# Optimization experiments

Hardware: AMD Instinct MI355X
Metric: run time of the kernel (lower is better)

## Reference

```python
import jax, jax.numpy as jnp
import numpy as np

N_EMBD = 1024
N_HEAD = 16
HEAD_DIM = N_EMBD // N_HEAD
D_FF = 4 * N_EMBD


def dyt(x, alpha, gamma, beta):
    # Dynamic Tanh normalizer: gamma * tanh(alpha * x) + beta
    return gamma * jnp.tanh(x * alpha) + beta


def setup_inputs() -> dict:
    key = jax.random.key(0)
    ks = jax.random.split(key, 9)
    C, F = N_EMBD, D_FF
    s = 0.02
    return {
        "x": jax.random.normal(ks[0], (2, 2048, C), dtype=jnp.float32),
        "alpha": jnp.ones((1,), jnp.float32) * 0.5,
        "gamma": jnp.ones((C,), jnp.float32),
        "beta": jnp.zeros((C,), jnp.float32),
        "w_attn": jax.random.normal(ks[1], (C, 3 * C), jnp.float32) * s,
        "b_attn": jnp.zeros((3 * C,), jnp.float32),
        "w_proj": jax.random.normal(ks[2], (C, C), jnp.float32) * s,
        "b_proj": jnp.zeros((C,), jnp.float32),
        "w_fc": jax.random.normal(ks[3], (C, F), jnp.float32) * s,
        "b_fc": jnp.zeros((F,), jnp.float32),
        "w_fc2": jax.random.normal(ks[4], (F, C), jnp.float32) * s,
        "b_fc2": jnp.zeros((C,), jnp.float32),
    }


def reference(x, alpha, gamma, beta, w_attn, b_attn, w_proj, b_proj,
              w_fc, b_fc, w_fc2, b_fc2):
    B, T, C = x.shape
    H, D = N_HEAD, HEAD_DIM

    # --- attention branch (pre-norm with DyT) ---
    h = dyt(x, alpha, gamma, beta)
    qkv = h @ w_attn + b_attn                      # [B,T,3C]
    q, k, v = jnp.split(qkv, 3, axis=-1)
    q = q.reshape(B, T, H, D).transpose(0, 2, 1, 3)  # [B,H,T,D]
    k = k.reshape(B, T, H, D).transpose(0, 2, 1, 3)
    v = v.reshape(B, T, H, D).transpose(0, 2, 1, 3)

    scores = jnp.einsum('bhqd,bhkd->bhqk', q, k) / jnp.sqrt(jnp.asarray(D, x.dtype))
    causal = jnp.tril(jnp.ones((T, T), bool))
    scores = jnp.where(causal[None, None], scores, -jnp.inf)
    attn = jax.nn.softmax(scores, axis=-1)          # [B,H,T,T]
    out = jnp.einsum('bhqk,bhkd->bhqd', attn, v)    # [B,H,T,D]
    out = out.transpose(0, 2, 1, 3).reshape(B, T, C)
    x = x + (out @ w_proj + b_proj)

    # --- MLP branch (pre-norm with same DyT params, as in source) ---
    h2 = dyt(x, alpha, gamma, beta)
    mlp = jax.nn.gelu(h2 @ w_fc + b_fc, approximate=False) @ w_fc2 + b_fc2
    return x + mlp
```

## Files before the change

### kernel.cpp

```cpp
#include <hip/hip_runtime.h>
#include <cstdint>
#include <cstddef>

typedef __bf16 bf16;
typedef __bf16 bf16x8 __attribute__((ext_vector_type(8)));
typedef __bf16 bf16x4 __attribute__((ext_vector_type(4)));
typedef float f32x4 __attribute__((ext_vector_type(4)));

#define DEVI __device__ __forceinline__

DEVI void gload_lds16(const bf16* g, bf16* l) {
    __builtin_amdgcn_global_load_lds(
        (const __attribute__((address_space(1))) void*)(const void*)g,
        (__attribute__((address_space(3))) void*)(void*)l, 16, 0, 0);
}

DEVI float fast_tanh(float y) {
    float t = __builtin_amdgcn_exp2f(2.88539008f * y);
    return 1.f - 2.f * __builtin_amdgcn_rcpf(1.f + t);
}

__global__ void conv_all_kernel(const float* __restrict__ wa, const float* __restrict__ wp,
                                const float* __restrict__ wfc, const float* __restrict__ wfc2,
                                bf16* __restrict__ ta, bf16* __restrict__ tp,
                                bf16* __restrict__ tfc, bf16* __restrict__ tfc2) {
    __shared__ float tile[64][65];
    int bid = blockIdx.x;
    const float* W; bf16* Wt; int K, N, nx;
    if (bid < 768)        { W = wa;   Wt = ta;   K = 1024; N = 3072; nx = 48; }
    else if (bid < 1024)  { bid -= 768;  W = wp;   Wt = tp;   K = 1024; N = 1024; nx = 16; }
    else if (bid < 2048)  { bid -= 1024; W = wfc;  Wt = tfc;  K = 1024; N = 4096; nx = 64; }
    else                  { bid -= 2048; W = wfc2; Wt = tfc2; K = 4096; N = 1024; nx = 16; }
    const int n0 = (bid % nx) * 64;
    const int k0 = (bid / nx) * 64;
    const int tid = threadIdx.x;
    const int c  = tid & 63;
    const int r4 = tid >> 6;
#pragma unroll
    for (int r = 0; r < 64; r += 4)
        tile[r + r4][c] = W[(size_t)(k0 + r + r4) * N + n0 + c];
    __syncthreads();
#pragma unroll
    for (int r = 0; r < 64; r += 4)
        Wt[(size_t)(n0 + r + r4) * K + k0 + c] = (bf16)tile[c][r + r4];
}

__global__ void dyt_kernel(const float* __restrict__ x, const float* __restrict__ alpha,
                           const float* __restrict__ gamma, const float* __restrict__ beta,
                           bf16* __restrict__ h, int total) {
    int i4 = (blockIdx.x * 256 + threadIdx.x) * 4;
    if (i4 >= total) return;
    float a = alpha[0];
    float4 xv = *(const float4*)&x[i4];
    int c = i4 & 1023;
    float4 g  = *(const float4*)&gamma[c];
    float4 bt = *(const float4*)&beta[c];
    bf16x4 o;
    o[0] = (bf16)(g.x * fast_tanh(xv.x * a) + bt.x);
    o[1] = (bf16)(g.y * fast_tanh(xv.y * a) + bt.y);
    o[2] = (bf16)(g.z * fast_tanh(xv.z * a) + bt.z);
    o[3] = (bf16)(g.w * fast_tanh(xv.w * a) + bt.w);
    *(bf16x4*)&h[i4] = o;
}

__global__ void reduce4_kernel(const bf16* __restrict__ p, const float* __restrict__ bias,
                               const bf16* __restrict__ x2b, float* __restrict__ out,
                               int total) {
    int i4 = (blockIdx.x * 256 + threadIdx.x) * 4;
    if (i4 >= total) return;
    bf16x4 q0 = *(const bf16x4*)&p[i4];
    bf16x4 q1 = *(const bf16x4*)&p[(size_t)total + i4];
    bf16x4 q2 = *(const bf16x4*)&p[(size_t)2 * total + i4];
    bf16x4 q3 = *(const bf16x4*)&p[(size_t)3 * total + i4];
    bf16x4 rr = *(const bf16x4*)&x2b[i4];
    int c = i4 & 1023;
    float4 bb = *(const float4*)&bias[c];
    float4 o;
    o.x = (float)q0[0] + (float)q1[0] + (float)q2[0] + (float)q3[0] + (float)rr[0] + bb.x;
    o.y = (float)q0[1] + (float)q1[1] + (float)q2[1] + (float)q3[1] + (float)rr[1] + bb.y;
    o.z = (float)q0[2] + (float)q1[2] + (float)q2[2] + (float)q3[2] + (float)rr[2] + bb.z;
    o.w = (float)q0[3] + (float)q1[3] + (float)q2[3] + (float)q3[3] + (float)rr[3] + bb.w;
    *(float4*)&out[i4] = o;
}

__global__ void reduce2b_dyt_kernel(const bf16* __restrict__ p, const float* __restrict__ bias,
                                    const float* __restrict__ x,
                                    bf16* __restrict__ x2b, bf16* __restrict__ hout,
                                    const float* __restrict__ alpha,
                                    const float* __restrict__ gamma,
                                    const float* __restrict__ beta, int total) {
    int i4 = (blockIdx.x * 256 + threadIdx.x) * 4;
    if (i4 >= total) return;
    float a = alpha[0];
    bf16x4 p0 = *(const bf16x4*)&p[i4];
    bf16x4 p1 = *(const bf16x4*)&p[(size_t)total + i4];
    float4 r  = *(const float4*)&x[i4];
    int c = i4 & 1023;
    float4 bb = *(const float4*)&bias[c];
    float4 g  = *(const float4*)&gamma[c];
    float4 bt = *(const float4*)&beta[c];
    float4 v;
    v.x = (float)p0[0] + (float)p1[0] + r.x + bb.x;
    v.y = (float)p0[1] + (float)p1[1] + r.y + bb.y;
    v.z = (float)p0[2] + (float)p1[2] + r.z + bb.z;
    v.w = (float)p0[3] + (float)p1[3] + r.w + bb.w;
    bf16x4 xo;
    xo[0] = (bf16)v.x; xo[1] = (bf16)v.y; xo[2] = (bf16)v.z; xo[3] = (bf16)v.w;
    *(bf16x4*)&x2b[i4] = xo;
    bf16x4 o;
    o[0] = (bf16)(g.x * fast_tanh(v.x * a) + bt.x);
    o[1] = (bf16)(g.y * fast_tanh(v.y * a) + bt.y);
    o[2] = (bf16)(g.z * fast_tanh(v.z * a) + bt.z);
    o[3] = (bf16)(g.w * fast_tanh(v.w * a) + bt.w);
    *(bf16x4*)&hout[i4] = o;
}

template<int OP>
__global__ void gemm_kernel(const bf16* __restrict__ A, const bf16* __restrict__ Wt,
                            const float* __restrict__ bias, const float* resid,
                            float* outf, bf16* outb,
                            const float* __restrict__ alpha_p,
                            const float* __restrict__ gamma,
                            const float* __restrict__ beta,
                            int M, int N, int K, int lda, int ldb) {
    __shared__ bf16 As[2][128 * 32];
    __shared__ bf16 Bs[2][128 * 32];
    const int tid  = threadIdx.x;
    const int lane = tid & 63;
    const int w    = tid >> 6;
    const int wr   = w >> 1, wc = w & 1;

    const int nwgx = gridDim.x;
    const int nwg  = gridDim.x * gridDim.y;
    const int orig = blockIdx.y * nwgx + blockIdx.x;
    const int cpx  = nwg >> 3;
    const int swz  = (orig & 7) * cpx + (orig >> 3);
    const int bm = (swz / nwgx) * 128;
    const int bn = (swz % nwgx) * 128;
    const int kz = blockIdx.z * K;

    f32x4 acc[4][4] = {};

    const int srow = tid >> 2;
    const int sgrp = ((tid & 3) ^ ((srow >> 1) & 3)) * 8;
    const bf16* a0 = A  + (size_t)(bm + srow) * lda + kz + sgrp;
    const bf16* a1 = a0 + (size_t)64 * lda;
    const bf16* b0 = Wt + (size_t)(bn + srow) * ldb + kz + sgrp;
    const bf16* b1 = b0 + (size_t)64 * ldb;

    auto stage = [&](int buf) {
        gload_lds16(a0, &As[buf][tid * 8]);
        gload_lds16(a1, &As[buf][2048 + tid * 8]);
        gload_lds16(b0, &Bs[buf][tid * 8]);
        gload_lds16(b1, &Bs[buf][2048 + tid * 8]);
        a0 += 32; a1 += 32; b0 += 32; b1 += 32;
    };

    const int lh = lane >> 4, lm = lane & 15;
    const int arow = wr * 64 + lm;
    const int brow = wc * 64 + lm;
    const int gsw = (lh ^ ((lm >> 1) & 3)) * 8;

    stage(0);
    __syncthreads();

    const int nk = K >> 5;
    for (int kt = 0; kt < nk; ++kt) {
        const int cur = kt & 1;
        if (kt + 1 < nk) stage(cur ^ 1);
        bf16x8 af[4], bfr[4];
#pragma unroll
        for (int i = 0; i < 4; i++)
            af[i] = *(const bf16x8*)&As[cur][(arow + i * 16) * 32 + gsw];
#pragma unroll
        for (int i = 0; i < 4; i++)
            bfr[i] = *(const bf16x8*)&Bs[cur][(brow + i * 16) * 32 + gsw];
#pragma unroll
        for (int i = 0; i < 4; i++)
#pragma unroll
            for (int j = 0; j < 4; j++)
                acc[i][j] = __builtin_amdgcn_mfma_f32_16x16x32_bf16(af[i], bfr[j], acc[i][j], 0, 0, 0);
        __syncthreads();
    }

#pragma unroll
    for (int i = 0; i < 4; i++) {
        const int row0 = bm + wr * 64 + i * 16 + lh * 4;
#pragma unroll
        for (int jf = 0; jf < 4; jf++) {
            const int col = bn + wc * 64 + jf * 16 + lm;
            const float bval = (OP == 5) ? 0.f : bias[col];
#pragma unroll
            for (int r = 0; r < 4; r++) {
                const int row = row0 + r;
                const size_t idx = (size_t)row * N + col;
                float v = acc[i][jf][r] + bval;
                if (OP == 0) {
                    const float qs = (col < 1024) ? 0.18033688011f : 1.0f;
                    outb[idx] = (bf16)(v * qs);
                } else {
                    outb[(size_t)blockIdx.z * M * N + idx] = (bf16)v;
                }
            }
        }
    }
}

template<int OP>
__global__ void __launch_bounds__(512, 2)
gemm256_kernel(const bf16* __restrict__ A, const bf16* __restrict__ Wt,
               const float* __restrict__ bias,
               bf16* __restrict__ outb, bf16* __restrict__ outpb,
               int M, int N, int K, int lda, int ldb) {
    __shared__ bf16 As[2][256][64];
    __shared__ bf16 Bs[2][256][64];
    const int tid  = threadIdx.x;
    const int lane = tid & 63;
    const int w    = tid >> 6;
    const int wr   = w >> 2;
    const int wcn  = w & 3;
    const int lh = lane >> 4, lm = lane & 15;

    const int nwgx = gridDim.x;
    const int nwg  = gridDim.x * gridDim.y;
    const int orig = blockIdx.y * nwgx + blockIdx.x;
    const int cpx  = nwg >> 3;
    const int swz  = (orig & 7) * cpx + (orig >> 3);
    const int bm = (swz / nwgx) * 256;
    const int bn = (swz % nwgx) * 256;
    const int kz = blockIdx.z * K;

    f32x4 acc[8][4] = {};

    const int srow = tid >> 3;
    const int sgr  = ((tid & 7) ^ (srow & 7)) * 8;
    const bf16* aSrc = A  + (size_t)(bm + srow) * lda + kz + sgr;
    const bf16* bSrc = Wt + (size_t)(bn + srow) * ldb + kz + sgr;

    auto STAGE = [&](int b, int kt) {
#pragma unroll
        for (int l = 0; l < 4; ++l)
            gload_lds16(aSrc + (size_t)(l * 64) * lda + kt * 64,
                        &As[b][0][0] + (l * 512 + tid) * 8);
#pragma unroll
        for (int l = 0; l < 4; ++l)
            gload_lds16(bSrc + (size_t)(l * 64) * ldb + kt * 64,
                        &Bs[b][0][0] + (l * 512 + tid) * 8);
    };

    auto COMPUTE2 = [&](int b) {
        bf16x8 bfr[2][2][2];
#pragma unroll
        for (int half = 0; half < 2; ++half) {
            bf16x8 af[4][2];
#pragma unroll
            for (int mf = 0; mf < 4; ++mf) {
                const int row = wr * 128 + (half * 4 + mf) * 16 + lm;
                const int sw = row & 7;
#pragma unroll
                for (int ks = 0; ks < 2; ++ks)
                    af[mf][ks] = *(const bf16x8*)&As[b][row][((ks * 4 + lh) ^ sw) * 8];
            }
            if (half == 0) {
#pragma unroll
                for (int qn = 0; qn < 2; ++qn)
#pragma unroll
                    for (int nf = 0; nf < 2; ++nf) {
                        const int row = wcn * 64 + (qn * 2 + nf) * 16 + lm;
                        const int sw = row & 7;
#pragma unroll
                        for (int ks = 0; ks < 2; ++ks)
                            bfr[qn][nf][ks] = *(const bf16x8*)&Bs[b][row][((ks * 4 + lh) ^ sw) * 8];
                    }
            }
            __builtin_amdgcn_s_setprio(1);
#pragma unroll
            for (int ks = 0; ks < 2; ++ks)
#pragma unroll
                for (int qn = 0; qn < 2; ++qn)
#pragma unroll
                    for (int mf = 0; mf < 4; ++mf)
#pragma unroll
                        for (int nf = 0; nf < 2; ++nf)
                            acc[half * 4 + mf][qn * 2 + nf] = __builtin_amdgcn_mfma_f32_16x16x32_bf16(
                                af[mf][ks], bfr[qn][nf][ks], acc[half * 4 + mf][qn * 2 + nf], 0, 0, 0);
            __builtin_amdgcn_s_setprio(0);
        }
    };

    const int nk = K >> 6;
    STAGE(0, 0);
    STAGE(1, 1);
    asm volatile("s_waitcnt vmcnt(8)" ::: "memory");
    __builtin_amdgcn_s_barrier();
    __builtin_amdgcn_sched_barrier(0);

    for (int kt = 0; kt < nk; kt += 2) {
        COMPUTE2(0);
        __builtin_amdgcn_s_barrier();
        if (kt + 2 < nk) {
            STAGE(0, kt + 2);
            asm volatile("s_waitcnt vmcnt(8)" ::: "memory");
        } else {
            asm volatile("s_waitcnt vmcnt(0)" ::: "memory");
        }
        __builtin_amdgcn_s_barrier();
        __builtin_amdgcn_sched_barrier(0);
        COMPUTE2(1);
        __builtin_amdgcn_s_barrier();
        if (kt + 3 < nk) {
            STAGE(1, kt + 3);
            asm volatile("s_waitcnt vmcnt(8)" ::: "memory");
        } else if (kt + 2 < nk) {
            asm volatile("s_waitcnt vmcnt(0)" ::: "memory");
        }
        __builtin_amdgcn_s_barrier();
        __builtin_amdgcn_sched_barrier(0);
    }

#pragma unroll
    for (int mf = 0; mf < 8; ++mf) {
        const int row0 = bm + wr * 128 + mf * 16 + lh * 4;
#pragma unroll
        for (int nf = 0; nf < 4; ++nf) {
            const int col = bn + wcn * 64 + nf * 16 + lm;
            const float bval = (OP == 4) ? 0.f : bias[col];
#pragma unroll
            for (int r = 0; r < 4; ++r) {
                const size_t idx = (size_t)(row0 + r) * N + col;
                float v = acc[mf][nf][r] + bval;
                if (OP == 2) {
                    float xc = v * (1.f + 0.044715f * v * v);
                    float g = v * __builtin_amdgcn_rcpf(
                        1.f + __builtin_amdgcn_exp2f(-2.30220795f * xc));
                    outb[idx] = (bf16)g;
                } else {
                    outpb[(size_t)blockIdx.z * M * N + idx] = (bf16)v;
                }
            }
        }
    }
}

__global__ void __launch_bounds__(256, 2)
attn_kernel(const bf16* __restrict__ qkv, bf16* __restrict__ out) {
    const int j  = blockIdx.x;
    const int bh = blockIdx.y;
    const int b = bh >> 4, h = bh & 15;
    const int tid = threadIdx.x, lane = tid & 63, w = tid >> 6;
    const int T = 2048;
    const size_t C3 = 3072;
    const bf16* qb = qkv + (size_t)b * T * C3 + h * 64;
    const bf16* kb = qb + 1024;
    const bf16* vb = qb + 2048;

    __shared__ bf16 Ks[2][64][64];
    __shared__ bf16 Vt[2][64][72];
    __shared__ bf16 Pl[2][4][16][72];

    const int tA = j, tB = 31 - j;
    const int qA = tA * 64 + w * 16;
    const int qB = tB * 64 + w * 16;
    const int lm = lane & 15;
    const int lh = lane >> 4;

    bf16x8 qfA0, qfA1, qfB0, qfB1;
    {
        size_t qo = (size_t)(qA + lm) * C3 + lh * 8;
        qfA0 = *(const bf16x8*)&qb[qo];
        qfA1 = *(const bf16x8*)&qb[qo + 32];
        qo = (size_t)(qB + lm) * C3 + lh * 8;
        qfB0 = *(const bf16x8*)&qb[qo];
        qfB1 = *(const bf16x8*)&qb[qo + 32];
    }
    f32x4 accA[4] = {}, accB[4] = {};
    float lA = 0.f, lB = 0.f;

    const int nt = tB + 1;
    const int sg = tid & 7;
    const int sq = tid >> 3;
    bf16x8 rv[4];

    const int krow = tid >> 3;
    const int kcb  = tid & 7;
    const int kcbs = (kcb ^ (krow & 7)) * 8;
    auto stageK = [&](int buf, int k0) {
        gload_lds16(&kb[(size_t)(k0 + krow) * C3 + kcbs],      &Ks[buf][0][0]  + tid * 8);
        gload_lds16(&kb[(size_t)(k0 + 32 + krow) * C3 + kcbs], &Ks[buf][32][0] + tid * 8);
    };
    auto loadV = [&](int k0) {
        if (tid < 128) {
#pragma unroll
            for (int i = 0; i < 4; ++i)
                rv[i] = *(const bf16x8*)&vb[(size_t)(k0 + sq * 4 + i) * C3 + sg * 8];
        }
    };
    auto writeV = [&](int buf) {
        if (tid < 128) {
            const int cbase = ((((sq >> 1) ^ sg) & 7) << 3) + ((sq & 1) << 2);
#pragma unroll
            for (int e = 0; e < 8; ++e) {
                bf16x4 wv;
                wv[0] = rv[0][e]; wv[1] = rv[1][e]; wv[2] = rv[2][e]; wv[3] = rv[3][e];
                *(bf16x4*)&Vt[buf][sg * 8 + e][cbase] = wv;
            }
        }
    };

    auto softmax_pv = [&](f32x4 (&s)[4], f32x4 (&acc)[4], float& lS,
                          int qg, bool diag, int k0, int slot, bf16x8 (&vf)[2][4]) {
        if (diag) {
#pragma unroll
            for (int f = 0; f < 4; ++f)
#pragma unroll
                for (int r = 0; r < 4; ++r) {
                    const int kgl = k0 + f * 16 + lh * 4 + r;
                    s[f][r] = (kgl > qg) ? -1e30f : s[f][r];
                }
        }
        float rs = 0.f;
#pragma unroll
        for (int f = 0; f < 4; ++f) {
            bf16x4 pw;
#pragma unroll
            for (int r = 0; r < 4; ++r) {
                const float pv = __builtin_amdgcn_exp2f(s[f][r]);
                rs += pv;
                pw[r] = (bf16)pv;
            }
            *(bf16x4*)&Pl[slot][w][lm][f * 16 + lh * 4] = pw;
        }
        __builtin_amdgcn_s_setprio(1);
#pragma unroll
        for (int kk = 0; kk < 2; ++kk) {
            bf16x8 pa = *(const bf16x8*)&Pl[slot][w][lm][kk * 32 + lh * 8];
#pragma unroll
            for (int df = 0; df < 4; ++df)
                acc[df] = __builtin_amdgcn_mfma_f32_16x16x32_bf16(vf[kk][df], pa, acc[df], 0, 0, 0);
        }
        __builtin_amdgcn_s_setprio(0);
        rs += __shfl_xor(rs, 16);
        rs += __shfl_xor(rs, 32);
        lS += rs;
    };

    stageK(0, 0);
    loadV(0);
    writeV(0);
    __syncthreads();

    for (int kt = 0; kt < nt; ++kt) {
        const int k0 = kt * 64;
        const int buf = kt & 1;
        const bool hasNext = (kt + 1 < nt);
        if (hasNext) {
            stageK(buf ^ 1, k0 + 64);
            loadV(k0 + 64);
        }

        bf16x8 kf[4][2];
#pragma unroll
        for (int f = 0; f < 4; ++f) {
            const int row = f * 16 + lm;
            const int sw = (row & 7);
            kf[f][0] = *(const bf16x8*)&Ks[buf][row][(lh ^ sw) * 8];
            kf[f][1] = *(const bf16x8*)&Ks[buf][row][((lh + 4) ^ sw) * 8];
        }
        bf16x8 vf[2][4];
#pragma unroll
        for (int kk = 0; kk < 2; ++kk)
#pragma unroll
            for (int df = 0; df < 4; ++df) {
                const int dr = df * 16 + lm;
                vf[kk][df] = *(const bf16x8*)&Vt[buf][dr][(((4 * kk + lh) ^ ((dr >> 3) & 7)) << 3)];
            }

        const bool actA = (kt <= tA);
        f32x4 sA[4], sB[4];
        __builtin_amdgcn_s_setprio(1);
#pragma unroll
        for (int f = 0; f < 4; ++f) {
            f32x4 z = {};
            z = __builtin_amdgcn_mfma_f32_16x16x32_bf16(kf[f][0], qfB0, z, 0, 0, 0);
            z = __builtin_amdgcn_mfma_f32_16x16x32_bf16(kf[f][1], qfB1, z, 0, 0, 0);
            sB[f] = z;
        }
        if (actA) {
#pragma unroll
            for (int f = 0; f < 4; ++f) {
                f32x4 z = {};
                z = __builtin_amdgcn_mfma_f32_16x16x32_bf16(kf[f][0], qfA0, z, 0, 0, 0);
                z = __builtin_amdgcn_mfma_f32_16x16x32_bf16(kf[f][1], qfA1, z, 0, 0, 0);
                sA[f] = z;
            }
        }
        __builtin_amdgcn_s_setprio(0);

        if (actA)
            softmax_pv(sA, accA, lA, qA + lm, kt == tA, k0, 0, vf);
        if (hasNext) writeV(buf ^ 1);
        softmax_pv(sB, accB, lB, qB + lm, kt == tB, k0, 1, vf);
        __syncthreads();
    }

    bf16* obase = out + (size_t)b * T * 1024 + h * 64;
    {
        const float linv = 1.0f / lA;
        bf16* ob = obase + (size_t)(qA + lm) * 1024;
#pragma unroll
        for (int df = 0; df < 4; ++df) {
            bf16x4 st;
#pragma unroll
            for (int r = 0; r < 4; ++r) st[r] = (bf16)(accA[df][r] * linv);
            *(bf16x4*)&ob[df * 16 + lh * 4] = st;
        }
    }
    {
        const float linv = 1.0f / lB;
        bf16* ob = obase + (size_t)(qB + lm) * 1024;
#pragma unroll
        for (int df = 0; df < 4; ++df) {
            bf16x4 st;
#pragma unroll
            for (int r = 0; r < 4; ++r) st[r] = (bf16)(accB[df][r] * linv);
            *(bf16x4*)&ob[df * 16 + lh * 4] = st;
        }
    }
}

extern "C" void kernel_launch(void* const* d_in, const int* in_sizes, int n_in,
                              void* d_out, int out_size, void* d_ws, size_t ws_size,
                              hipStream_t stream) {
    const float* x      = (const float*)d_in[0];
    const float* alpha  = (const float*)d_in[1];
    const float* gamma  = (const float*)d_in[2];
    const float* beta   = (const float*)d_in[3];
    const float* w_attn = (const float*)d_in[4];
    const float* b_attn = (const float*)d_in[5];
    const float* w_proj = (const float*)d_in[6];
    const float* b_proj = (const float*)d_in[7];
    const float* w_fc   = (const float*)d_in[8];
    const float* b_fc   = (const float*)d_in[9];
    const float* w_fc2  = (const float*)d_in[10];
    const float* b_fc2  = (const float*)d_in[11];
    float* out = (float*)d_out;

    const int M = 4096, C = 1024, F = 4096;
    char* ws = (char*)d_ws;
    bf16* wt_attn = (bf16*)ws;
    bf16* wt_proj = wt_attn + (size_t)3 * C * C;
    bf16* wt_fc   = wt_proj + (size_t)C * C;
    bf16* wt_fc2  = wt_fc   + (size_t)F * C;
    bf16* hbuf    = wt_fc2  + (size_t)C * F;
    bf16* qkvbuf  = hbuf    + (size_t)M * C;
    bf16* aout    = qkvbuf  + (size_t)M * F;
    bf16* x2b     = aout    + (size_t)M * C;
    bf16* part4   = x2b     + (size_t)M * C;
    const size_t need = (size_t)(80 + 32) * 1024 * 1024;
    const bool splitK = ws_size >= need;

    dim3 blk(256);
    conv_all_kernel<<<dim3(3072), blk, 0, stream>>>(
        w_attn, w_proj, w_fc, w_fc2, wt_attn, wt_proj, wt_fc, wt_fc2);

    dyt_kernel<<<dim3(M * C / 1024), blk, 0, stream>>>(x, alpha, gamma, beta, hbuf, M * C);

    gemm_kernel<0><<<dim3(3 * C / 128, M / 128), blk, 0, stream>>>(
        hbuf, wt_attn, b_attn, nullptr, nullptr, qkvbuf, nullptr, nullptr, nullptr,
        M, 3 * C, C, C, C);

    attn_kernel<<<dim3(16, 32), blk, 0, stream>>>(qkvbuf, aout);

    gemm_kernel<5><<<dim3(C / 128, M / 128, 2), blk, 0, stream>>>(
        aout, wt_proj, b_proj, nullptr, nullptr, part4, nullptr, nullptr, nullptr,
        M, C, C / 2, C, C);
    reduce2b_dyt_kernel<<<dim3(M * C / 1024), blk, 0, stream>>>(
        part4, b_proj, x, x2b, hbuf, alpha, gamma, beta, M * C);

    gemm256_kernel<2><<<dim3(F / 256, M / 256), dim3(512), 0, stream>>>(
        hbuf, wt_fc, b_fc, qkvbuf, nullptr, M, F, C, C, C);

    gemm256_kernel<4><<<dim3(C / 256, M / 256, 4), dim3(512), 0, stream>>>(
        qkvbuf, wt_fc2, b_fc2, nullptr, part4, M, C, F / 4, F, F);
    reduce4_kernel<<<dim3(M * C / 1024), blk, 0, stream>>>(part4, b_fc2, x2b, out, M * C);
    (void)splitK;
}
```

Baseline: 212.2 us.

## Split attention key loop across two interleaved partitions with fp32 combine kernel

The attention kernel now runs a third grid dimension of two splits. Each split handles alternating 64-key tiles and writes unnormalized fp32 partial outputs plus row sums. A new combine kernel adds the two partials, normalizes them and writes the bf16 attention output. This doubles the number of blocks to raise parallelism and shorten each block's serial key loop. The cost is an extra kernel launch and extra fp32 traffic to global memory for the partial outputs.

```diff
diff --git a/kernel.cpp b/kernel.cpp
--- a/kernel.cpp
+++ b/kernel.cpp
@@ -61,6 +61,26 @@
     o[2] = (bf16)(g.z * fast_tanh(xv.z * a) + bt.z);
     o[3] = (bf16)(g.w * fast_tanh(xv.w * a) + bt.w);
     *(bf16x4*)&h[i4] = o;
+}
+
+__global__ void attn_combine_kernel(const float* __restrict__ po, const float* __restrict__ pl,
+                                    bf16* __restrict__ aout, int total) {
+    int i4 = (blockIdx.x * 256 + threadIdx.x) * 4;
+    if (i4 >= total) return;
+    const int row = i4 >> 10;
+    const int c = i4 & 1023;
+    const int b = row >> 11, t = row & 2047, h = c >> 6;
+    const int li = ((b * 16 + h) << 11) + t;
+    const float l0 = pl[li], l1 = pl[65536 + li];
+    const float inv = __builtin_amdgcn_rcpf(l0 + l1);
+    float4 o0 = *(const float4*)&po[i4];
+    float4 o1 = *(const float4*)&po[(size_t)total + i4];
+    bf16x4 o;
+    o[0] = (bf16)((o0.x + o1.x) * inv);
+    o[1] = (bf16)((o0.y + o1.y) * inv);
+    o[2] = (bf16)((o0.z + o1.z) * inv);
+    o[3] = (bf16)((o0.w + o1.w) * inv);
+    *(bf16x4*)&aout[i4] = o;
 }
 
 __global__ void reduce4_kernel(const bf16* __restrict__ p, const float* __restrict__ bias,
@@ -343,9 +363,11 @@
 }
 
 __global__ void __launch_bounds__(256, 2)
-attn_kernel(const bf16* __restrict__ qkv, bf16* __restrict__ out) {
+attn_kernel(const bf16* __restrict__ qkv, float* __restrict__ po,
+            float* __restrict__ pl) {
     const int j  = blockIdx.x;
     const int bh = blockIdx.y;
+    const int z  = blockIdx.z;
     const int b = bh >> 4, h = bh & 15;
     const int tid = threadIdx.x, lane = tid & 63, w = tid >> 6;
     const int T = 2048;
@@ -376,7 +398,6 @@
     f32x4 accA[4] = {}, accB[4] = {};
     float lA = 0.f, lB = 0.f;
 
-    const int nt = tB + 1;
     const int sg = tid & 7;
     const int sq = tid >> 3;
     bf16x8 rv[4];
@@ -444,18 +465,19 @@
         lS += rs;
     };
 
-    stageK(0, 0);
-    loadV(0);
+    stageK(0, z * 64);
+    loadV(z * 64);
     writeV(0);
     __syncthreads();
 
-    for (int kt = 0; kt < nt; ++kt) {
+    int it = 0;
+    for (int kt = z; kt <= tB; kt += 2, ++it) {
         const int k0 = kt * 64;
-        const int buf = kt & 1;
-        const bool hasNext = (kt + 1 < nt);
+        const int buf = it & 1;
+        const bool hasNext = (kt + 2 <= tB);
         if (hasNext) {
-            stageK(buf ^ 1, k0 + 64);
-            loadV(k0 + 64);
+            stageK(buf ^ 1, k0 + 128);
+            loadV(k0 + 128);
         }
 
         bf16x8 kf[4][2];
@@ -480,18 +502,18 @@
         __builtin_amdgcn_s_setprio(1);
 #pragma unroll
         for (int f = 0; f < 4; ++f) {
-            f32x4 z = {};
-            z = __builtin_amdgcn_mfma_f32_16x16x32_bf16(kf[f][0], qfB0, z, 0, 0, 0);
-            z = __builtin_amdgcn_mfma_f32_16x16x32_bf16(kf[f][1], qfB1, z, 0, 0, 0);
-            sB[f] = z;
+            f32x4 zz = {};
+            zz = __builtin_amdgcn_mfma_f32_16x16x32_bf16(kf[f][0], qfB0, zz, 0, 0, 0);
+            zz = __builtin_amdgcn_mfma_f32_16x16x32_bf16(kf[f][1], qfB1, zz, 0, 0, 0);
+            sB[f] = zz;
         }
         if (actA) {
 #pragma unroll
             for (int f = 0; f < 4; ++f) {
-                f32x4 z = {};
-                z = __builtin_amdgcn_mfma_f32_16x16x32_bf16(kf[f][0], qfA0, z, 0, 0, 0);
-                z = __builtin_amdgcn_mfma_f32_16x16x32_bf16(kf[f][1], qfA1, z, 0, 0, 0);
-                sA[f] = z;
+                f32x4 zz = {};
+                zz = __builtin_amdgcn_mfma_f32_16x16x32_bf16(kf[f][0], qfA0, zz, 0, 0, 0);
+                zz = __builtin_amdgcn_mfma_f32_16x16x32_bf16(kf[f][1], qfA1, zz, 0, 0, 0);
+                sA[f] = zz;
             }
         }
         __builtin_amdgcn_s_setprio(0);
@@ -503,28 +525,21 @@
         __syncthreads();
     }
 
-    bf16* obase = out + (size_t)b * T * 1024 + h * 64;
+    const size_t MC = (size_t)4096 * 1024;
+    float* pobase = po + (size_t)z * MC + (size_t)b * T * 1024 + h * 64;
     {
-        const float linv = 1.0f / lA;
-        bf16* ob = obase + (size_t)(qA + lm) * 1024;
-#pragma unroll
-        for (int df = 0; df < 4; ++df) {
-            bf16x4 st;
-#pragma unroll
-            for (int r = 0; r < 4; ++r) st[r] = (bf16)(accA[df][r] * linv);
-            *(bf16x4*)&ob[df * 16 + lh * 4] = st;
-        }
+        float* ob = pobase + (size_t)(qA + lm) * 1024;
+#pragma unroll
+        for (int df = 0; df < 4; ++df)
+            *(f32x4*)&ob[df * 16 + lh * 4] = accA[df];
+        if (lh == 0) pl[z * 65536 + (bh << 11) + qA + lm] = lA;
     }
     {
-        const float linv = 1.0f / lB;
-        bf16* ob = obase + (size_t)(qB + lm) * 1024;
-#pragma unroll
-        for (int df = 0; df < 4; ++df) {
-            bf16x4 st;
-#pragma unroll
-            for (int r = 0; r < 4; ++r) st[r] = (bf16)(accB[df][r] * linv);
-            *(bf16x4*)&ob[df * 16 + lh * 4] = st;
-        }
+        float* ob = pobase + (size_t)(qB + lm) * 1024;
+#pragma unroll
+        for (int df = 0; df < 4; ++df)
+            *(f32x4*)&ob[df * 16 + lh * 4] = accB[df];
+        if (lh == 0) pl[z * 65536 + (bh << 11) + qB + lm] = lB;
     }
 }
 
@@ -556,8 +571,8 @@
     bf16* aout    = qkvbuf  + (size_t)M * F;
     bf16* x2b     = aout    + (size_t)M * C;
     bf16* part4   = x2b     + (size_t)M * C;
-    const size_t need = (size_t)(80 + 32) * 1024 * 1024;
-    const bool splitK = ws_size >= need;
+    float* po     = (float*)part4;
+    float* pl     = (float*)(part4 + (size_t)4 * M * C);
 
     dim3 blk(256);
     conv_all_kernel<<<dim3(3072), blk, 0, stream>>>(
@@ -569,7 +584,8 @@
         hbuf, wt_attn, b_attn, nullptr, nullptr, qkvbuf, nullptr, nullptr, nullptr,
         M, 3 * C, C, C, C);
 
-    attn_kernel<<<dim3(16, 32), blk, 0, stream>>>(qkvbuf, aout);
+    attn_kernel<<<dim3(16, 32, 2), blk, 0, stream>>>(qkvbuf, po, pl);
+    attn_combine_kernel<<<dim3(M * C / 1024), blk, 0, stream>>>(po, pl, aout, M * C);
 
     gemm_kernel<5><<<dim3(C / 128, M / 128, 2), blk, 0, stream>>>(
         aout, wt_proj, b_proj, nullptr, nullptr, part4, nullptr, nullptr, nullptr,
@@ -583,5 +599,4 @@
     gemm256_kernel<4><<<dim3(C / 256, M / 256, 4), dim3(512), 0, stream>>>(
         qkvbuf, wt_fc2, b_fc2, nullptr, part4, M, C, F / 4, F, F);
     reduce4_kernel<<<dim3(M * C / 1024), blk, 0, stream>>>(part4, b_fc2, x2b, out, M * C);
-    (void)splitK;
-}
+}
```

Measured after the change: 229.7 us. 1.08x slower.
